# Kernel tuning notes

Measured on AMD Instinct MI355X. Metric: run time of the kernel, lower is better.

The kernel has to match this reference:

```python
import jax, jax.numpy as jnp
import numpy as np

B, S, H = 4, 2048, 1024
NH, HD = 16, 64
ROPE_THETA = 160000.0
SCALE = HD ** -0.5


def _rope_cos_sin(position_ids, dim, theta):
    # neox-style rotary: frequencies over half the head dim
    inv_freq = 1.0 / (theta ** (jnp.arange(0, dim, 2, dtype=jnp.float32) / dim))  # [dim/2]
    freqs = position_ids.astype(jnp.float32)[..., None] * inv_freq  # [B,S,dim/2]
    return jnp.cos(freqs), jnp.sin(freqs)


def _apply_rope(x, cos, sin):
    # x: [B,S,NH,HD]; neox style: rotate halves
    d2 = x.shape[-1] // 2
    x1, x2 = x[..., :d2], x[..., d2:]
    c = cos[:, :, None, :]
    s = sin[:, :, None, :]
    return jnp.concatenate([x1 * c - x2 * s, x2 * c + x1 * s], axis=-1)


def setup_inputs() -> dict:
    key = jax.random.key(0)
    k1, k2, k3 = jax.random.split(key, 3)
    hidden_states = jax.random.normal(k1, (B, S, H), dtype=jnp.float32)
    position_ids = jnp.tile(jnp.arange(S, dtype=jnp.int32)[None, :], (B, 1))
    Wqkv = jax.random.normal(k2, (3 * H, H), dtype=jnp.float32) * (H ** -0.5)
    Wo = jax.random.normal(k3, (H, H), dtype=jnp.float32) * (H ** -0.5)
    return {"hidden_states": hidden_states, "position_ids": position_ids,
            "Wqkv": Wqkv, "Wo": Wo}


def reference(hidden_states, position_ids, Wqkv, Wo):
    # fused QKV projection
    qkv = jnp.einsum('bsh,oh->bso', hidden_states, Wqkv)  # [B,S,3H]
    q, k, v = jnp.split(qkv, 3, axis=-1)
    q = q.reshape(B, S, NH, HD)
    k = k.reshape(B, S, NH, HD)
    v = v.reshape(B, S, NH, HD)
    # rotary embedding (neox style)
    cos, sin = _rope_cos_sin(position_ids, HD, ROPE_THETA)
    q = _apply_rope(q, cos, sin)
    k = _apply_rope(k, cos, sin)
    # full bidirectional (encoder-only, global layer) attention
    scores = jnp.einsum('bqhd,bkhd->bhqk', q, k) * SCALE  # [B,NH,S,S]
    probs = jax.nn.softmax(scores, axis=-1)
    ctx = jnp.einsum('bhqk,bkhd->bqhd', probs, v).reshape(B, S, H)
    # output projection
    return jnp.einsum('bsh,oh->bso', ctx, Wo)
```

## Files before the change

### kernel.cpp

```cpp
#include <hip/hip_runtime.h>
#include <hip/hip_bf16.h>


#define GLOBAL_AS __attribute__((address_space(1)))
#define LDS_AS    __attribute__((address_space(3)))

using f32x4 = __attribute__((ext_vector_type(4))) float;
using s16x8 = __attribute__((ext_vector_type(8))) short;

__device__ __forceinline__ void gld_lds16(const void* g, void* l) {
  __builtin_amdgcn_global_load_lds((const GLOBAL_AS void*)g, (LDS_AS void*)l, 16, 0, 0);
}

__device__ __forceinline__ unsigned short f2bf(float f) {
  unsigned int u = __float_as_uint(f);
  u = (u + 0x7fffu + ((u >> 16) & 1u)) >> 16;
  return (unsigned short)u;
}
__device__ __forceinline__ unsigned int cvt_pk_bf16(float lo, float hi) {
  unsigned int r;
  asm("v_cvt_pk_bf16_f32 %0, %1, %2" : "=v"(r) : "v"(lo), "v"(hi));
  return r;
}

__global__ __launch_bounds__(256) void cvt_all_kernel(const float* __restrict__ h,
                                                      const float* __restrict__ wq,
                                                      const float* __restrict__ wo,
                                                      unsigned short* __restrict__ hb,
                                                      unsigned short* __restrict__ wqb,
                                                      unsigned short* __restrict__ wob) {
  int b = blockIdx.x;
  const float* src; unsigned short* dst; int i;
  if (b < 8192)       { src = h;  dst = hb;  i = b * 256 + threadIdx.x; }
  else if (b < 11264) { src = wq; dst = wqb; i = (b - 8192) * 256 + threadIdx.x; }
  else                { src = wo; dst = wob; i = (b - 11264) * 256 + threadIdx.x; }
  float4 v = ((const float4*)src)[i];
  ushort4 o;
  o.x = f2bf(v.x); o.y = f2bf(v.y); o.z = f2bf(v.z); o.w = f2bf(v.w);
  ((ushort4*)dst)[i] = o;
}

__global__ __launch_bounds__(256) void rope_table_kernel(const int* __restrict__ pos,
                                                         float* __restrict__ ctab,
                                                         float* __restrict__ stab) {
  int idx = blockIdx.x * 256 + threadIdx.x;
  int d = idx & 31;
  int bs = idx >> 5;
  float p = (float)pos[bs];
  float inv = exp2f(-(float)d * 0.5402410118609203f);
  float f = p * inv;
  ctab[idx] = cosf(f);
  stab[idx] = sinf(f);
}

template<int MODE>
__global__ __launch_bounds__(256) void gemm_bt_kernel(const unsigned short* __restrict__ A,
                                                      const unsigned short* __restrict__ Bm,
                                                      void* __restrict__ C, int N, int K,
                                                      const float* __restrict__ ctab,
                                                      const float* __restrict__ stab,
                                                      unsigned short* __restrict__ Qr,
                                                      unsigned short* __restrict__ Kr,
                                                      unsigned short* __restrict__ vbuf) {
  __shared__ char sA[16384];
  __shared__ char sB[16384];
  const int tid  = threadIdx.x;
  const int lane = tid & 63, w = tid >> 6;
  const int g = lane >> 4, c = lane & 15;
  const int wr = w >> 1, wc = w & 1;
  const int m0 = blockIdx.x * 128, n0 = blockIdx.y * 128;
  const char* Ab = (const char*)A;
  const char* Bb = (const char*)Bm;

  f32x4 acc[4][4] = {};
  for (int k0 = 0; k0 < K; k0 += 64) {
    __syncthreads();
#pragma unroll
    for (int rr = 0; rr < 4; ++rr) {
      int o = tid * 16 + rr * 4096;
      int row = o >> 7;
      int col = (o & 127) ^ ((row & 7) << 4);
      gld_lds16(Ab + ((size_t)(m0 + row) * K + k0) * 2 + col, sA + o);
      gld_lds16(Bb + ((size_t)(n0 + row) * K + k0) * 2 + col, sB + o);
    }
    __syncthreads();
#pragma unroll
    for (int ks = 0; ks < 2; ++ks) {
      s16x8 af[4], bfr[4];
#pragma unroll
      for (int i = 0; i < 4; ++i) {
        int row = 64 * wr + 16 * i + c;
        af[i] = *(const s16x8*)(sA + ((row * 128 + ks * 64 + g * 16) ^ ((row & 7) << 4)));
      }
#pragma unroll
      for (int j = 0; j < 4; ++j) {
        int row = 64 * wc + 16 * j + c;
        bfr[j] = *(const s16x8*)(sB + ((row * 128 + ks * 64 + g * 16) ^ ((row & 7) << 4)));
      }
#pragma unroll
      for (int i = 0; i < 4; ++i)
#pragma unroll
        for (int j = 0; j < 4; ++j)
          acc[i][j] = __builtin_amdgcn_mfma_f32_16x16x32_bf16(af[i], bfr[j], acc[i][j], 0, 0, 0);
    }
  }

  if (MODE == 1) {
#pragma unroll
    for (int i = 0; i < 4; ++i)
#pragma unroll
      for (int j = 0; j < 4; ++j)
#pragma unroll
        for (int r = 0; r < 4; ++r) {
          int m = m0 + 64 * wr + 16 * i + 4 * g + r;
          int n = n0 + 64 * wc + 16 * j + c;
          ((float*)C)[(size_t)m * N + n] = acc[i][j][r];
        }
  } else {
    const int t = blockIdx.y;
    if (t < 16) {
      unsigned short* dstb = (t < 8) ? Qr : Kr;
      const float qs = (t < 8) ? 0.18033688011112042f : 1.0f;
      const int h = 2 * (t & 7) + wc;
#pragma unroll
      for (int i = 0; i < 4; ++i)
#pragma unroll
        for (int r = 0; r < 4; ++r) {
          int m = m0 + 64 * wr + 16 * i + 4 * g + r;
          int b = m >> 11, s = m & 2047;
          unsigned short* drow = dstb + ((size_t)(b * 16 + h) * 2048 + s) * 64;
#pragma unroll
          for (int j = 0; j < 2; ++j) {
            int d = 16 * j + c;
            float co = ctab[(size_t)m * 32 + d];
            float si = stab[(size_t)m * 32 + d];
            float x1 = acc[i][j][r], x2 = acc[i][j + 2][r];
            drow[d]      = f2bf((x1 * co - x2 * si) * qs);
            drow[d + 32] = f2bf((x2 * co + x1 * si) * qs);
          }
        }
    } else {
#pragma unroll
      for (int i = 0; i < 4; ++i)
#pragma unroll
        for (int j = 0; j < 4; ++j)
#pragma unroll
          for (int r = 0; r < 4; ++r) {
            int m = m0 + 64 * wr + 16 * i + 4 * g + r;
            int n = (t - 16) * 128 + 64 * wc + 16 * j + c;
            vbuf[(size_t)m * 1024 + n] = f2bf(acc[i][j][r]);
          }
    }
  }
}

__global__ __launch_bounds__(256) void vtrans_kernel(const unsigned short* __restrict__ vbuf,
                                                     unsigned short* __restrict__ Vt) {
  __shared__ unsigned short tile[64][80];
  int bid = blockIdx.x;
  int st = bid & 31, h = (bid >> 5) & 15, b = bid >> 9;
  int s0 = st * 64;
  int t = threadIdx.x;
  {
    int row = t >> 2, part = t & 3;
    const unsigned short* src = vbuf + ((size_t)(b * 2048 + s0 + row)) * 1024 + h * 64 + part * 16;
    uint4 v0 = *(const uint4*)(src);
    uint4 v1 = *(const uint4*)(src + 8);
    *(uint4*)&tile[row][part * 16]     = v0;
    *(uint4*)&tile[row][part * 16 + 8] = v1;
  }
  __syncthreads();
  {
    int d = t >> 2, sp = t & 3;
    unsigned short vals[16];
#pragma unroll
    for (int i = 0; i < 16; ++i) vals[i] = tile[sp * 16 + i][d];
    unsigned short* dst = Vt + ((size_t)(b * 16 + h) * 64 + d) * 2048 + s0 + sp * 16;
    *(uint4*)(dst)     = ((const uint4*)vals)[0];
    *(uint4*)(dst + 8) = ((const uint4*)vals)[1];
  }
}

__global__ __launch_bounds__(256, 3) void attn_kernel(const unsigned short* __restrict__ Q,
                                                      const unsigned short* __restrict__ Kr,
                                                      const unsigned short* __restrict__ Vt,
                                                      unsigned short* __restrict__ Ctx) {
  __shared__ char sK[2][8192];
  __shared__ char sV[2][8192];
  __shared__ char sP[8192];
  const int tid  = threadIdx.x;
  const int lane = tid & 63, w = tid >> 6;
  const int g = lane >> 4, c = lane & 15;
  int lin = blockIdx.x + 16 * blockIdx.y;
  int eff = (lin & 7) * 128 + (lin >> 3);
  const int bh = eff >> 4;
  const int q0 = (eff & 15) * 128;
  const char* kh = (const char*)(Kr + (size_t)bh * 2048 * 64);
  const char* vh = (const char*)(Vt + (size_t)bh * 64 * 2048);

  s16x8 qf[2][2];
#pragma unroll
  for (int u = 0; u < 2; ++u) {
    const char* qrow = (const char*)(Q + (size_t)bh * 2048 * 64) + (size_t)(q0 + 32 * w + 16 * u + c) * 128;
    qf[u][0] = *(const s16x8*)(qrow + g * 16);
    qf[u][1] = *(const s16x8*)(qrow + 64 + g * 16);
  }

#pragma unroll
  for (int rr = 0; rr < 2; ++rr) {
    int o = tid * 16 + rr * 4096;
    int l = o ^ (((o >> 7) & 7) << 4);
    gld_lds16(kh + l, sK[0] + o);
    gld_lds16(vh + (size_t)(o >> 7) * 4096 + (l & 127), sV[0] + o);
  }

  float l_run[2] = {0.f, 0.f};
  f32x4 o_acc[2][4] = {};
  char* pw = sP + w * 2048;

  for (int it = 0; it < 32; ++it) {
    __syncthreads();
    const int cur = it & 1;
    if (it + 1 < 32) {
      int kvn = (it + 1) * 64;
#pragma unroll
      for (int rr = 0; rr < 2; ++rr) {
        int o = tid * 16 + rr * 4096;
        int l = o ^ (((o >> 7) & 7) << 4);
        gld_lds16(kh + (size_t)kvn * 128 + l, sK[cur ^ 1] + o);
        gld_lds16(vh + (size_t)(o >> 7) * 4096 + kvn * 2 + (l & 127), sV[cur ^ 1] + o);
      }
    }

    __builtin_amdgcn_s_setprio(1);
    f32x4 sc0[4] = {}, sc1[4] = {};
#pragma unroll
    for (int j = 0; j < 4; ++j) {
      int row = 16 * j + c;
#pragma unroll
      for (int ks = 0; ks < 2; ++ks) {
        s16x8 kb = *(const s16x8*)(sK[cur] + ((row * 128 + ks * 64 + g * 16) ^ ((c & 7) << 4)));
        sc0[j] = __builtin_amdgcn_mfma_f32_16x16x32_bf16(kb, qf[0][ks], sc0[j], 0, 0, 0);
        sc1[j] = __builtin_amdgcn_mfma_f32_16x16x32_bf16(kb, qf[1][ks], sc1[j], 0, 0, 0);
      }
    }
    __builtin_amdgcn_s_setprio(0);

    {
      float rs = 0.f;
#pragma unroll
      for (int j = 0; j < 4; ++j) {
        float e0 = __builtin_amdgcn_exp2f(sc0[j][0]);
        float e1 = __builtin_amdgcn_exp2f(sc0[j][1]);
        float e2 = __builtin_amdgcn_exp2f(sc0[j][2]);
        float e3 = __builtin_amdgcn_exp2f(sc0[j][3]);
        rs += (e0 + e1) + (e2 + e3);
        uint2 pk;
        pk.x = cvt_pk_bf16(e0, e1);
        pk.y = cvt_pk_bf16(e2, e3);
        *(uint2*)(pw + ((c * 128 + 32 * j + 8 * g) ^ ((c & 7) << 4))) = pk;
      }
      l_run[0] += rs;
    }
    asm volatile("s_waitcnt lgkmcnt(0)" ::: "memory");
    __builtin_amdgcn_s_setprio(1);
#pragma unroll
    for (int ns = 0; ns < 2; ++ns) {
      s16x8 pa = *(const s16x8*)(pw + ((c * 128 + ns * 64 + g * 16) ^ ((c & 7) << 4)));
#pragma unroll
      for (int dj = 0; dj < 4; ++dj) {
        int row = 16 * dj + c;
        s16x8 vb = *(const s16x8*)(sV[cur] + ((row * 128 + ns * 64 + g * 16) ^ ((c & 7) << 4)));
        o_acc[0][dj] = __builtin_amdgcn_mfma_f32_16x16x32_bf16(pa, vb, o_acc[0][dj], 0, 0, 0);
      }
    }
    __builtin_amdgcn_s_setprio(0);
    asm volatile("" ::: "memory");

    {
      float rs = 0.f;
#pragma unroll
      for (int j = 0; j < 4; ++j) {
        float e0 = __builtin_amdgcn_exp2f(sc1[j][0]);
        float e1 = __builtin_amdgcn_exp2f(sc1[j][1]);
        float e2 = __builtin_amdgcn_exp2f(sc1[j][2]);
        float e3 = __builtin_amdgcn_exp2f(sc1[j][3]);
        rs += (e0 + e1) + (e2 + e3);
        uint2 pk;
        pk.x = cvt_pk_bf16(e0, e1);
        pk.y = cvt_pk_bf16(e2, e3);
        *(uint2*)(pw + ((c * 128 + 32 * j + 8 * g) ^ ((c & 7) << 4))) = pk;
      }
      l_run[1] += rs;
    }
    asm volatile("s_waitcnt lgkmcnt(0)" ::: "memory");
    __builtin_amdgcn_s_setprio(1);
#pragma unroll
    for (int ns = 0; ns < 2; ++ns) {
      s16x8 pa = *(const s16x8*)(pw + ((c * 128 + ns * 64 + g * 16) ^ ((c & 7) << 4)));
#pragma unroll
      for (int dj = 0; dj < 4; ++dj) {
        int row = 16 * dj + c;
        s16x8 vb = *(const s16x8*)(sV[cur] + ((row * 128 + ns * 64 + g * 16) ^ ((c & 7) << 4)));
        o_acc[1][dj] = __builtin_amdgcn_mfma_f32_16x16x32_bf16(pa, vb, o_acc[1][dj], 0, 0, 0);
      }
    }
    __builtin_amdgcn_s_setprio(0);
    asm volatile("" ::: "memory");
  }

  const int b = bh >> 4, h = bh & 15;
#pragma unroll
  for (int u = 0; u < 2; ++u) {
    float l = l_run[u];
    l += __shfl_xor(l, 16);
    l += __shfl_xor(l, 32);
#pragma unroll
    for (int r = 0; r < 4; ++r) {
      float lr = __shfl(l, (lane & 48) | (4 * g + r));
      float inv = 1.f / lr;
      int srow = q0 + 32 * w + 16 * u + 4 * g + r;
      unsigned short* crow = Ctx + ((size_t)(b * 2048 + srow)) * 1024 + h * 64;
#pragma unroll
      for (int dj = 0; dj < 4; ++dj)
        crow[16 * dj + c] = f2bf(o_acc[u][dj][r] * inv);
    }
  }
}

extern "C" void kernel_launch(void* const* d_in, const int* in_sizes, int n_in,
                              void* d_out, int out_size, void* d_ws, size_t ws_size,
                              hipStream_t stream) {
  const float* hidden = (const float*)d_in[0];
  const int*   pos    = (const int*)d_in[1];
  const float* wqkv   = (const float*)d_in[2];
  const float* wo     = (const float*)d_in[3];

  char* ws = (char*)d_ws;
  unsigned short* hbf  = (unsigned short*)(ws);
  unsigned short* wqbf = (unsigned short*)(ws + 16777216);
  unsigned short* wobf = (unsigned short*)(ws + 23068672);
  unsigned short* vbuf = (unsigned short*)(ws + 25165824);
  unsigned short* Qr   = (unsigned short*)(ws + 41943040);
  unsigned short* Kr   = (unsigned short*)(ws + 58720256);
  unsigned short* Vt   = (unsigned short*)(ws + 75497472);
  unsigned short* ctx  = (unsigned short*)(ws + 92274688);
  float*          ctab = (float*)(ws + 109051904);
  float*          stab = (float*)(ws + 110100480);

  cvt_all_kernel<<<12288, 256, 0, stream>>>(hidden, wqkv, wo, hbf, wqbf, wobf);
  rope_table_kernel<<<1024, 256, 0, stream>>>(pos, ctab, stab);

  dim3 gq(64, 24);
  gemm_bt_kernel<2><<<gq, 256, 0, stream>>>(hbf, wqbf, nullptr, 3072, 1024,
                                            ctab, stab, Qr, Kr, vbuf);

  vtrans_kernel<<<2048, 256, 0, stream>>>(vbuf, Vt);

  dim3 ga(16, 64);
  attn_kernel<<<ga, 256, 0, stream>>>(Qr, Kr, Vt, ctx);

  dim3 go(64, 8);
  gemm_bt_kernel<1><<<go, 256, 0, stream>>>(ctx, wobf, d_out, 1024, 1024,
                                            nullptr, nullptr, nullptr, nullptr, nullptr);
}
```

Before: 213.3 us.

## Use 32x32x16 MFMA in attention and keep P in registers via permlane swap

Rewrites the attention inner loop to use 32x32x16 bf16 MFMAs with K and V as the A operand, so each lane owns one query row. The exponentiated scores are converted to bf16 and rearranged with v_permlane32_swap, so they feed the PV MFMA straight from registers. This removes the LDS round-trip for P and the waitcnt stalls around it. The occupancy hint of 3 blocks per SM is dropped and the accumulators grow to 16-wide vectors, which may raise register pressure. The epilogue now writes vectorized 4-element stores per row.

```diff
diff --git a/kernel.cpp b/kernel.cpp
--- a/kernel.cpp
+++ b/kernel.cpp
@@ -5,8 +5,9 @@
 #define GLOBAL_AS __attribute__((address_space(1)))
 #define LDS_AS    __attribute__((address_space(3)))
 
-using f32x4 = __attribute__((ext_vector_type(4))) float;
-using s16x8 = __attribute__((ext_vector_type(8))) short;
+using f32x4  = __attribute__((ext_vector_type(4))) float;
+using f32x16 = __attribute__((ext_vector_type(16))) float;
+using s16x8  = __attribute__((ext_vector_type(8))) short;
 
 __device__ __forceinline__ void gld_lds16(const void* g, void* l) {
   __builtin_amdgcn_global_load_lds((const GLOBAL_AS void*)g, (LDS_AS void*)l, 16, 0, 0);
@@ -21,6 +22,9 @@
   unsigned int r;
   asm("v_cvt_pk_bf16_f32 %0, %1, %2" : "=v"(r) : "v"(lo), "v"(hi));
   return r;
+}
+__device__ __forceinline__ void pswap(unsigned int& a, unsigned int& b) {
+  asm("v_permlane32_swap_b32 %0, %1" : "+v"(a), "+v"(b));
 }
 
 __global__ __launch_bounds__(256) void cvt_all_kernel(const float* __restrict__ h,
@@ -181,16 +185,16 @@
   }
 }
 
-__global__ __launch_bounds__(256, 3) void attn_kernel(const unsigned short* __restrict__ Q,
-                                                      const unsigned short* __restrict__ Kr,
-                                                      const unsigned short* __restrict__ Vt,
-                                                      unsigned short* __restrict__ Ctx) {
+__global__ __launch_bounds__(256) void attn_kernel(const unsigned short* __restrict__ Q,
+                                                   const unsigned short* __restrict__ Kr,
+                                                   const unsigned short* __restrict__ Vt,
+                                                   unsigned short* __restrict__ Ctx) {
   __shared__ char sK[2][8192];
   __shared__ char sV[2][8192];
-  __shared__ char sP[8192];
   const int tid  = threadIdx.x;
   const int lane = tid & 63, w = tid >> 6;
-  const int g = lane >> 4, c = lane & 15;
+  const int hi = lane >> 5, ql = lane & 31;
+  const int swz = (ql & 7) << 4;
   int lin = blockIdx.x + 16 * blockIdx.y;
   int eff = (lin & 7) * 128 + (lin >> 3);
   const int bh = eff >> 4;
@@ -198,12 +202,11 @@
   const char* kh = (const char*)(Kr + (size_t)bh * 2048 * 64);
   const char* vh = (const char*)(Vt + (size_t)bh * 64 * 2048);
 
-  s16x8 qf[2][2];
-#pragma unroll
-  for (int u = 0; u < 2; ++u) {
-    const char* qrow = (const char*)(Q + (size_t)bh * 2048 * 64) + (size_t)(q0 + 32 * w + 16 * u + c) * 128;
-    qf[u][0] = *(const s16x8*)(qrow + g * 16);
-    qf[u][1] = *(const s16x8*)(qrow + 64 + g * 16);
+  s16x8 qf[4];
+  {
+    const char* qrow = (const char*)Q + ((size_t)bh * 2048 + q0 + 32 * w + ql) * 128;
+#pragma unroll
+    for (int t = 0; t < 4; ++t) qf[t] = *(const s16x8*)(qrow + t * 32 + hi * 16);
   }
 
 #pragma unroll
@@ -214,9 +217,8 @@
     gld_lds16(vh + (size_t)(o >> 7) * 4096 + (l & 127), sV[0] + o);
   }
 
-  float l_run[2] = {0.f, 0.f};
-  f32x4 o_acc[2][4] = {};
-  char* pw = sP + w * 2048;
+  float l_run = 0.f;
+  f32x16 oa0 = {}, oa1 = {};
 
   for (int it = 0; it < 32; ++it) {
     __syncthreads();
@@ -232,98 +234,75 @@
       }
     }
 
+    f32x16 sc0 = {}, sc1 = {};
     __builtin_amdgcn_s_setprio(1);
-    f32x4 sc0[4] = {}, sc1[4] = {};
-#pragma unroll
-    for (int j = 0; j < 4; ++j) {
-      int row = 16 * j + c;
-#pragma unroll
-      for (int ks = 0; ks < 2; ++ks) {
-        s16x8 kb = *(const s16x8*)(sK[cur] + ((row * 128 + ks * 64 + g * 16) ^ ((c & 7) << 4)));
-        sc0[j] = __builtin_amdgcn_mfma_f32_16x16x32_bf16(kb, qf[0][ks], sc0[j], 0, 0, 0);
-        sc1[j] = __builtin_amdgcn_mfma_f32_16x16x32_bf16(kb, qf[1][ks], sc1[j], 0, 0, 0);
-      }
+#pragma unroll
+    for (int t = 0; t < 4; ++t) {
+      int cx = (t * 32 + hi * 16) ^ swz;
+      s16x8 k0 = *(const s16x8*)(sK[cur] + ql * 128 + cx);
+      s16x8 k1 = *(const s16x8*)(sK[cur] + (32 + ql) * 128 + cx);
+      sc0 = __builtin_amdgcn_mfma_f32_32x32x16_bf16(k0, qf[t], sc0, 0, 0, 0);
+      sc1 = __builtin_amdgcn_mfma_f32_32x32x16_bf16(k1, qf[t], sc1, 0, 0, 0);
     }
     __builtin_amdgcn_s_setprio(0);
 
-    {
-      float rs = 0.f;
-#pragma unroll
-      for (int j = 0; j < 4; ++j) {
-        float e0 = __builtin_amdgcn_exp2f(sc0[j][0]);
-        float e1 = __builtin_amdgcn_exp2f(sc0[j][1]);
-        float e2 = __builtin_amdgcn_exp2f(sc0[j][2]);
-        float e3 = __builtin_amdgcn_exp2f(sc0[j][3]);
-        rs += (e0 + e1) + (e2 + e3);
-        uint2 pk;
-        pk.x = cvt_pk_bf16(e0, e1);
-        pk.y = cvt_pk_bf16(e2, e3);
-        *(uint2*)(pw + ((c * 128 + 32 * j + 8 * g) ^ ((c & 7) << 4))) = pk;
-      }
-      l_run[0] += rs;
-    }
-    asm volatile("s_waitcnt lgkmcnt(0)" ::: "memory");
+    float rs = 0.f;
+#pragma unroll
+    for (int r = 0; r < 16; ++r) { sc0[r] = __builtin_amdgcn_exp2f(sc0[r]); rs += sc0[r]; }
+#pragma unroll
+    for (int r = 0; r < 16; ++r) { sc1[r] = __builtin_amdgcn_exp2f(sc1[r]); rs += sc1[r]; }
+    l_run += rs;
+
+    unsigned int bp[16];
+#pragma unroll
+    for (int blk = 0; blk < 2; ++blk) {
+      const f32x16& s = blk ? sc1 : sc0;
+      unsigned int a0 = cvt_pk_bf16(s[0],  s[1]);
+      unsigned int a1 = cvt_pk_bf16(s[2],  s[3]);
+      unsigned int a2 = cvt_pk_bf16(s[4],  s[5]);
+      unsigned int a3 = cvt_pk_bf16(s[6],  s[7]);
+      pswap(a0, a2); pswap(a1, a3);
+      bp[blk * 8 + 0] = a0; bp[blk * 8 + 1] = a1;
+      bp[blk * 8 + 2] = a2; bp[blk * 8 + 3] = a3;
+      unsigned int b0 = cvt_pk_bf16(s[8],  s[9]);
+      unsigned int b1 = cvt_pk_bf16(s[10], s[11]);
+      unsigned int b2 = cvt_pk_bf16(s[12], s[13]);
+      unsigned int b3 = cvt_pk_bf16(s[14], s[15]);
+      pswap(b0, b2); pswap(b1, b3);
+      bp[blk * 8 + 4] = b0; bp[blk * 8 + 5] = b1;
+      bp[blk * 8 + 6] = b2; bp[blk * 8 + 7] = b3;
+    }
+
     __builtin_amdgcn_s_setprio(1);
 #pragma unroll
-    for (int ns = 0; ns < 2; ++ns) {
-      s16x8 pa = *(const s16x8*)(pw + ((c * 128 + ns * 64 + g * 16) ^ ((c & 7) << 4)));
-#pragma unroll
-      for (int dj = 0; dj < 4; ++dj) {
-        int row = 16 * dj + c;
-        s16x8 vb = *(const s16x8*)(sV[cur] + ((row * 128 + ns * 64 + g * 16) ^ ((c & 7) << 4)));
-        o_acc[0][dj] = __builtin_amdgcn_mfma_f32_16x16x32_bf16(pa, vb, o_acc[0][dj], 0, 0, 0);
-      }
+    for (int ss = 0; ss < 4; ++ss) {
+      uint4 u = {bp[ss * 4], bp[ss * 4 + 1], bp[ss * 4 + 2], bp[ss * 4 + 3]};
+      s16x8 pb = __builtin_bit_cast(s16x8, u);
+      int cx = (ss * 32 + hi * 16) ^ swz;
+      s16x8 v0 = *(const s16x8*)(sV[cur] + ql * 128 + cx);
+      s16x8 v1 = *(const s16x8*)(sV[cur] + (32 + ql) * 128 + cx);
+      oa0 = __builtin_amdgcn_mfma_f32_32x32x16_bf16(v0, pb, oa0, 0, 0, 0);
+      oa1 = __builtin_amdgcn_mfma_f32_32x32x16_bf16(v1, pb, oa1, 0, 0, 0);
     }
     __builtin_amdgcn_s_setprio(0);
-    asm volatile("" ::: "memory");
-
-    {
-      float rs = 0.f;
-#pragma unroll
-      for (int j = 0; j < 4; ++j) {
-        float e0 = __builtin_amdgcn_exp2f(sc1[j][0]);
-        float e1 = __builtin_amdgcn_exp2f(sc1[j][1]);
-        float e2 = __builtin_amdgcn_exp2f(sc1[j][2]);
-        float e3 = __builtin_amdgcn_exp2f(sc1[j][3]);
-        rs += (e0 + e1) + (e2 + e3);
-        uint2 pk;
-        pk.x = cvt_pk_bf16(e0, e1);
-        pk.y = cvt_pk_bf16(e2, e3);
-        *(uint2*)(pw + ((c * 128 + 32 * j + 8 * g) ^ ((c & 7) << 4))) = pk;
-      }
-      l_run[1] += rs;
-    }
-    asm volatile("s_waitcnt lgkmcnt(0)" ::: "memory");
-    __builtin_amdgcn_s_setprio(1);
-#pragma unroll
-    for (int ns = 0; ns < 2; ++ns) {
-      s16x8 pa = *(const s16x8*)(pw + ((c * 128 + ns * 64 + g * 16) ^ ((c & 7) << 4)));
-#pragma unroll
-      for (int dj = 0; dj < 4; ++dj) {
-        int row = 16 * dj + c;
-        s16x8 vb = *(const s16x8*)(sV[cur] + ((row * 128 + ns * 64 + g * 16) ^ ((c & 7) << 4)));
-        o_acc[1][dj] = __builtin_amdgcn_mfma_f32_16x16x32_bf16(pa, vb, o_acc[1][dj], 0, 0, 0);
-      }
-    }
-    __builtin_amdgcn_s_setprio(0);
-    asm volatile("" ::: "memory");
-  }
-
+  }
+
+  l_run += __shfl_xor(l_run, 32);
+  float inv = 1.f / l_run;
   const int b = bh >> 4, h = bh & 15;
-#pragma unroll
-  for (int u = 0; u < 2; ++u) {
-    float l = l_run[u];
-    l += __shfl_xor(l, 16);
-    l += __shfl_xor(l, 32);
-#pragma unroll
-    for (int r = 0; r < 4; ++r) {
-      float lr = __shfl(l, (lane & 48) | (4 * g + r));
-      float inv = 1.f / lr;
-      int srow = q0 + 32 * w + 16 * u + 4 * g + r;
-      unsigned short* crow = Ctx + ((size_t)(b * 2048 + srow)) * 1024 + h * 64;
-#pragma unroll
-      for (int dj = 0; dj < 4; ++dj)
-        crow[16 * dj + c] = f2bf(o_acc[u][dj][r] * inv);
+  const int q = q0 + 32 * w + ql;
+  unsigned short* crow = Ctx + ((size_t)(b * 2048 + q)) * 1024 + h * 64;
+#pragma unroll
+  for (int dblk = 0; dblk < 2; ++dblk) {
+    const f32x16& oa = dblk ? oa1 : oa0;
+#pragma unroll
+    for (int grp = 0; grp < 4; ++grp) {
+      ushort4 st;
+      st.x = f2bf(oa[4 * grp + 0] * inv);
+      st.y = f2bf(oa[4 * grp + 1] * inv);
+      st.z = f2bf(oa[4 * grp + 2] * inv);
+      st.w = f2bf(oa[4 * grp + 3] * inv);
+      *(ushort4*)(crow + dblk * 32 + 8 * grp + 4 * hi) = st;
     }
   }
 }
```

Measured after the change: 211.8 us. No clear change (-0.7%).
